# Optimization experiments

Hardware: AMD Instinct MI355X
Metric: run time of the kernel (lower is better)

## Reference

```python
import jax, jax.numpy as jnp
import numpy as np

N_USERS = 100_000
N_ENTITIES = 200_000
N_EDGES = 1_000_000
NNZ = 1_000_000
C = 64          # embedding dim
N_FACTORS = 4
N_REL_M1 = 10   # n_relations - 1
N_HOPS = 2
TEMP = 0.2


def setup_inputs() -> dict:
    key = jax.random.key(0)
    ks = jax.random.split(key, 10)
    return {
        'user_emb': jax.random.normal(ks[0], (N_USERS, C), jnp.float32) * 0.1,
        'entity_emb': jax.random.normal(ks[1], (N_ENTITIES, C), jnp.float32) * 0.1,
        'latent_emb': jax.random.normal(ks[2], (N_FACTORS, C), jnp.float32) * 0.1,
        'weight': jax.random.normal(ks[3], (N_REL_M1, C), jnp.float32) * 0.1,
        'disen_weight_att': jax.random.normal(ks[4], (N_FACTORS, N_REL_M1), jnp.float32) * 0.1,
        'edge_index': jax.random.randint(ks[5], (2, N_EDGES), 0, N_ENTITIES, dtype=jnp.int32),
        'edge_type': jax.random.randint(ks[6], (N_EDGES,), 1, N_REL_M1 + 1, dtype=jnp.int32),
        'inter_rows': jax.random.randint(ks[7], (NNZ,), 0, N_USERS, dtype=jnp.int32),
        'inter_cols': jax.random.randint(ks[8], (NNZ,), 0, N_ENTITIES, dtype=jnp.int32),
        'inter_vals': jax.random.uniform(ks[9], (NNZ,), jnp.float32),
    }


def _l2norm(x):
    # F.normalize(x, dim=1) with eps=1e-12
    n = jnp.linalg.norm(x, axis=1, keepdims=True)
    return x / jnp.maximum(n, 1e-12)


def _mutual_information(disen_weight_att):
    disen_T = disen_weight_att.T                                    # [R-1, F]
    nd = disen_T / jnp.linalg.norm(disen_T, axis=1, keepdims=True)
    pos_scores = jnp.sum(nd * nd, axis=1)
    ttl_scores = jnp.sum(disen_T @ disen_weight_att, axis=1)
    pos = jnp.exp(pos_scores / TEMP)
    ttl = jnp.exp(ttl_scores / TEMP)
    return -jnp.sum(jnp.log(pos / ttl))


def reference(user_emb, entity_emb, latent_emb, weight, disen_weight_att,
              edge_index, edge_type, inter_rows, inter_cols, inter_vals):
    entity_res = entity_emb
    user_res = user_emb
    cor = _mutual_information(disen_weight_att)

    head, tail = edge_index[0], edge_index[1]
    # edge degree for scatter_mean (constant across hops)
    cnt = jax.ops.segment_sum(jnp.ones((N_EDGES,), jnp.float32), head,
                              num_segments=N_ENTITIES)
    inv_cnt = 1.0 / jnp.maximum(cnt, 1.0)

    for _ in range(N_HOPS):
        # KG aggregate: gather tail entities, modulate by relation, scatter-mean to head
        rel = weight[edge_type - 1]                                  # [E, C]
        neigh = entity_emb[tail] * rel                               # [E, C]
        entity_agg = jax.ops.segment_sum(neigh, head, num_segments=N_ENTITIES)
        entity_agg = entity_agg * inv_cnt[:, None]

        # user -> latent factor attention
        score = jax.nn.softmax(user_emb @ latent_emb.T, axis=1)[:, :, None]  # [U, F, 1]

        # sparse user aggregate: interact_mat @ entity_emb
        user_agg = jax.ops.segment_sum(inter_vals[:, None] * entity_emb[inter_cols],
                                       inter_rows, num_segments=N_USERS)     # [U, C]

        disen_weight = jax.nn.softmax(disen_weight_att, axis=-1) @ weight    # [F, C]
        user_agg = user_agg * jnp.sum(disen_weight[None] * score, axis=1) + user_agg

        entity_emb = _l2norm(entity_agg)
        user_emb = _l2norm(user_agg)
        entity_res = entity_res + entity_emb
        user_res = user_res + user_emb

    return entity_res, user_res, cor
```

## Files before the change

kernel.cpp:

```cpp
#include <hip/hip_runtime.h>
#include <math.h>

#define N_USERS    100000
#define N_ENTITIES 200000
#define N_EDGES    1000000
#define NNZ        1000000
#define CDIM       64
#define N_FACTORS  4
#define N_REL      10
#define TEMP       0.2f

#define CB         1024
#define NBE        196
#define NBU        98
#define CAPE       8192
#define CAPU       12288
#define ACHUNK     4096
#define GA         245
#define GCVT       6250
#define KG_BLOCKS  6250
#define USER_BLOCKS 3125
#define PCHUNK     4096
#define GPE        49
#define GPU_       25

typedef unsigned int u32;
typedef unsigned short u16;
typedef unsigned char u8;

#if defined(__has_builtin)
#if __has_builtin(__builtin_amdgcn_cvt_pk_f32_fp8) && __has_builtin(__builtin_amdgcn_cvt_pk_fp8_f32)
#define HAVE_HW_FP8 1
#endif
#endif

__device__ __forceinline__ float bflo(u32 w) { return __uint_as_float(w << 16); }
__device__ __forceinline__ float bfhi(u32 w) { return __uint_as_float(w & 0xFFFF0000u); }
__device__ __forceinline__ u16 f2bf(float f) {
    u32 u = __float_as_uint(f);
    u32 r = u + 0x7FFFu + ((u >> 16) & 1u);
    return (u16)(r >> 16);
}
__device__ __forceinline__ void unpack8_bf(uint4 rv, float* x) {
    x[0] = bflo(rv.x); x[1] = bfhi(rv.x);
    x[2] = bflo(rv.y); x[3] = bfhi(rv.y);
    x[4] = bflo(rv.z); x[5] = bfhi(rv.z);
    x[6] = bflo(rv.w); x[7] = bfhi(rv.w);
}
__device__ __forceinline__ uint4 pack8_bf(const float* x) {
    uint4 o;
    o.x = (u32)f2bf(x[0]) | ((u32)f2bf(x[1]) << 16);
    o.y = (u32)f2bf(x[2]) | ((u32)f2bf(x[3]) << 16);
    o.z = (u32)f2bf(x[4]) | ((u32)f2bf(x[5]) << 16);
    o.w = (u32)f2bf(x[6]) | ((u32)f2bf(x[7]) << 16);
    return o;
}

#ifndef HAVE_HW_FP8
__device__ __forceinline__ float fp8_dec1(u32 b) {
    u32 s = b >> 7, em = b & 0x7F;
    float mag;
    if (em < 8) mag = (float)em * 0.001953125f;
    else {
        u32 bits = (((em >> 3) + 120u) << 23) | ((em & 7u) << 20);
        mag = __uint_as_float(bits);
    }
    return s ? -mag : mag;
}
__device__ __forceinline__ u32 fp8_enc1(float f) {
    float a = fabsf(f);
    u32 s = (__float_as_uint(f) >> 31) << 7;
    if (a < 0.015625f) {
        int n = (int)rintf(a * 512.0f);
        return s | (u32)n;
    }
    u32 u = __float_as_uint(a);
    u32 r = u + 0x0007FFFFu + ((u >> 20) & 1u);
    int ee = (int)((r >> 23) & 0xFF) - 127 + 7;
    if (ee >= 16) return s | 0x7Eu;
    return s | ((u32)ee << 3) | ((r >> 20) & 7u);
}
#endif

__device__ __forceinline__ void unpack8_fp8(uint2 rv, float* x) {
#ifdef HAVE_HW_FP8
    typedef float floatx2 __attribute__((ext_vector_type(2)));
    floatx2 a0 = __builtin_amdgcn_cvt_pk_f32_fp8(rv.x, false);
    floatx2 a1 = __builtin_amdgcn_cvt_pk_f32_fp8(rv.x, true);
    floatx2 a2 = __builtin_amdgcn_cvt_pk_f32_fp8(rv.y, false);
    floatx2 a3 = __builtin_amdgcn_cvt_pk_f32_fp8(rv.y, true);
    x[0] = a0.x; x[1] = a0.y; x[2] = a1.x; x[3] = a1.y;
    x[4] = a2.x; x[5] = a2.y; x[6] = a3.x; x[7] = a3.y;
#else
    x[0] = fp8_dec1(rv.x & 0xFF);         x[1] = fp8_dec1((rv.x >> 8) & 0xFF);
    x[2] = fp8_dec1((rv.x >> 16) & 0xFF); x[3] = fp8_dec1(rv.x >> 24);
    x[4] = fp8_dec1(rv.y & 0xFF);         x[5] = fp8_dec1((rv.y >> 8) & 0xFF);
    x[6] = fp8_dec1((rv.y >> 16) & 0xFF); x[7] = fp8_dec1(rv.y >> 24);
#endif
}
__device__ __forceinline__ uint2 pack8_fp8(const float* x) {
    uint2 o;
#ifdef HAVE_HW_FP8
    int v0 = 0, v1 = 0;
    v0 = __builtin_amdgcn_cvt_pk_fp8_f32(x[0], x[1], v0, false);
    v0 = __builtin_amdgcn_cvt_pk_fp8_f32(x[2], x[3], v0, true);
    v1 = __builtin_amdgcn_cvt_pk_fp8_f32(x[4], x[5], v1, false);
    v1 = __builtin_amdgcn_cvt_pk_fp8_f32(x[6], x[7], v1, true);
    o.x = (u32)v0; o.y = (u32)v1;
#else
    o.x = fp8_enc1(x[0]) | (fp8_enc1(x[1]) << 8) | (fp8_enc1(x[2]) << 16) | (fp8_enc1(x[3]) << 24);
    o.y = fp8_enc1(x[4]) | (fp8_enc1(x[5]) << 8) | (fp8_enc1(x[6]) << 16) | (fp8_enc1(x[7]) << 24);
#endif
    return o;
}

__device__ __forceinline__ void fma_rowW(float* acc, uint2 rv, int rel,
                                         const float* __restrict__ weight, int seg) {
    float x[8]; unpack8_fp8(rv, x);
    const float4* wp = (const float4*)(weight + rel * CDIM + seg * 8);
    float4 w0 = wp[0], w1 = wp[1];
    acc[0] += x[0] * w0.x; acc[1] += x[1] * w0.y;
    acc[2] += x[2] * w0.z; acc[3] += x[3] * w0.w;
    acc[4] += x[4] * w1.x; acc[5] += x[5] * w1.y;
    acc[6] += x[6] * w1.z; acc[7] += x[7] * w1.w;
}
__device__ __forceinline__ void fma_rowV(float* acc, uint2 rv, float v) {
    float x[8]; unpack8_fp8(rv, x);
    #pragma unroll
    for (int k = 0; k < 8; ++k) acc[k] += v * x[k];
}

__device__ void dev_cvt(int b, const float* __restrict__ in, u8* __restrict__ out) {
    int i = b * 256 + threadIdx.x;
    const float4* p = (const float4*)(in + (size_t)i * 8);
    float4 a = p[0], bb = p[1];
    float x[8] = {a.x, a.y, a.z, a.w, bb.x, bb.y, bb.z, bb.w};
    *(uint2*)(out + (size_t)i * 8) = pack8_fp8(x);
}

__device__ void dev_bin_edges(int b, const int* __restrict__ head,
                              const int* __restrict__ tail, const int* __restrict__ etype,
                              int* __restrict__ zcur, int* __restrict__ binbuf) {
    __shared__ int lh[256], lbase[256];
    int t = threadIdx.x;
    lh[t] = 0; __syncthreads();
    int base = b * ACHUNK;
    int rec[16], rnk[16], bkt[16];
    #pragma unroll
    for (int k = 0; k < 16; ++k) {
        int i = base + k * 256 + t;
        rnk[k] = -1; rec[k] = 0; bkt[k] = 0;
        if (i < N_EDGES) {
            int h = head[i];
            bkt[k] = h >> 10;
            rec[k] = ((h & 1023) << 22) | ((etype[i] - 1) << 18) | tail[i];
            rnk[k] = atomicAdd(&lh[bkt[k]], 1);
        }
    }
    __syncthreads();
    lbase[t] = lh[t] ? (t * CAPE + atomicAdd(&zcur[t], lh[t])) : 0;
    __syncthreads();
    #pragma unroll
    for (int k = 0; k < 16; ++k)
        if (rnk[k] >= 0) binbuf[lbase[bkt[k]] + rnk[k]] = rec[k];
}

__device__ void dev_bin_inter(int b, const int* __restrict__ rows,
                              const int* __restrict__ cols, const float* __restrict__ vals,
                              int* __restrict__ zcur, int2* __restrict__ binbuf) {
    __shared__ int lh[256], lbase[256];
    int t = threadIdx.x;
    lh[t] = 0; __syncthreads();
    int base = b * ACHUNK;
    int recx[16], recy[16], rnk[16], bkt[16];
    #pragma unroll
    for (int k = 0; k < 16; ++k) {
        int i = base + k * 256 + t;
        rnk[k] = -1; recx[k] = 0; recy[k] = 0; bkt[k] = 0;
        if (i < NNZ) {
            int r = rows[i];
            bkt[k] = r >> 10;
            recx[k] = ((r & 1023) << 18) | cols[i];
            recy[k] = __float_as_int(vals[i]);
            rnk[k] = atomicAdd(&lh[bkt[k]], 1);
        }
    }
    __syncthreads();
    lbase[t] = lh[t] ? (t * CAPU + atomicAdd(&zcur[t], lh[t])) : 0;
    __syncthreads();
    #pragma unroll
    for (int k = 0; k < 16; ++k)
        if (rnk[k] >= 0) {
            int2 p; p.x = recx[k]; p.y = recy[k];
            binbuf[lbase[bkt[k]] + rnk[k]] = p;
        }
}

__device__ void dev_disen_cor(const float* __restrict__ att,
                              const float* __restrict__ weight,
                              float* __restrict__ dw, float* __restrict__ cor_out) {
    int tid = threadIdx.x;
    int f = tid >> 6, c = tid & 63;
    float m = -1e30f;
    for (int r = 0; r < N_REL; ++r) m = fmaxf(m, att[f * N_REL + r]);
    float e[N_REL], s = 0.0f;
    for (int r = 0; r < N_REL; ++r) { e[r] = __expf(att[f * N_REL + r] - m); s += e[r]; }
    float acc = 0.0f;
    for (int r = 0; r < N_REL; ++r) acc += (e[r] / s) * weight[r * CDIM + c];
    dw[f * CDIM + c] = acc;

    if (tid == 0) {
        float rowsum[N_FACTORS];
        for (int ff = 0; ff < N_FACTORS; ++ff) {
            float ss = 0.0f;
            for (int j = 0; j < N_REL; ++j) ss += att[ff * N_REL + j];
            rowsum[ff] = ss;
        }
        float cor = 0.0f;
        for (int i = 0; i < N_REL; ++i) {
            float nsq = 0.0f, ttl = 0.0f;
            for (int ff = 0; ff < N_FACTORS; ++ff) {
                float a = att[ff * N_REL + i];
                nsq += a * a;
                ttl += a * rowsum[ff];
            }
            float n = sqrtf(nsq);
            float pos = 0.0f;
            for (int ff = 0; ff < N_FACTORS; ++ff) {
                float a = att[ff * N_REL + i] / n;
                pos += a * a;
            }
            cor += (ttl - pos) / TEMP;
        }
        *cor_out = cor;
    }
}

__global__ __launch_bounds__(256) void prep_kernel(const float* __restrict__ entity_emb,
                                                   u8* __restrict__ ef8,
                                                   const int* __restrict__ head,
                                                   const int* __restrict__ tail,
                                                   const int* __restrict__ etype,
                                                   const int* __restrict__ rows,
                                                   const int* __restrict__ cols,
                                                   const float* __restrict__ vals,
                                                   int* __restrict__ zce, int* __restrict__ zcu,
                                                   int* __restrict__ bine, int2* __restrict__ binu,
                                                   const float* __restrict__ att,
                                                   const float* __restrict__ weight,
                                                   float* __restrict__ dw,
                                                   float* __restrict__ cor_out) {
    int bid = blockIdx.x;
    if (bid < GCVT)                 dev_cvt(bid, entity_emb, ef8);
    else if (bid < GCVT + GA)       dev_bin_edges(bid - GCVT, head, tail, etype, zce, bine);
    else if (bid < GCVT + 2 * GA)   dev_bin_inter(bid - GCVT - GA, rows, cols, vals, zcu, binu);
    else                            dev_disen_cor(att, weight, dw, cor_out);
}

__device__ void dev_build_e(int b, const int* __restrict__ zce,
                            const int* __restrict__ binbuf,
                            int2* __restrict__ einfo, int* __restrict__ epk,
                            int* __restrict__ dbinE) {
    __shared__ int lh[CB];
    __shared__ int ss[256];
    __shared__ int ldeg[64];
    int t = threadIdx.x;
    int bstart = b * CAPE;
    int bend = bstart + zce[b];
    #pragma unroll
    for (int k = 0; k < 4; ++k) lh[t * 4 + k] = 0;
    if (t < 64) ldeg[t] = 0;
    __syncthreads();
    for (int j = bstart + t; j < bend; j += 256)
        atomicAdd(&lh[(u32)binbuf[j] >> 22], 1);
    __syncthreads();
    int v[4], acc = 0;
    #pragma unroll
    for (int k = 0; k < 4; ++k) { v[k] = lh[t * 4 + k]; acc += v[k]; }
    ss[t] = acc; __syncthreads();
    #pragma unroll
    for (int d = 1; d < 256; d <<= 1) {
        int x = (t >= d) ? ss[t - d] : 0;
        __syncthreads();
        ss[t] += x;
        __syncthreads();
    }
    int excl = ss[t] - acc;
    int hbase = b * CB;
    #pragma unroll
    for (int k = 0; k < 4; ++k) {
        int hl = t * 4 + k;
        int h = hbase + hl;
        if (h < N_ENTITIES) {
            int2 inf; inf.x = bstart + excl; inf.y = v[k];
            einfo[h] = inf;
            atomicAdd(&ldeg[63 - min(v[k], 63)], 1);
        }
        lh[hl] = excl;
        excl += v[k];
    }
    __syncthreads();
    if (t < 64 && ldeg[t]) atomicAdd(&dbinE[t], ldeg[t]);
    for (int j = bstart + t; j < bend; j += 256) {
        int rec = binbuf[j];
        int pos = atomicAdd(&lh[(u32)rec >> 22], 1);
        epk[bstart + pos] = rec & 0x3FFFFF;
    }
}

__device__ void dev_build_u(int b, const int* __restrict__ zcu,
                            const int2* __restrict__ binbuf,
                            int2* __restrict__ uinfo, int2* __restrict__ ucv,
                            int* __restrict__ dbinU) {
    __shared__ int lh[CB];
    __shared__ int ss[256];
    __shared__ int ldeg[64];
    int t = threadIdx.x;
    int bstart = b * CAPU;
    int bend = bstart + zcu[b];
    #pragma unroll
    for (int k = 0; k < 4; ++k) lh[t * 4 + k] = 0;
    if (t < 64) ldeg[t] = 0;
    __syncthreads();
    for (int j = bstart + t; j < bend; j += 256)
        atomicAdd(&lh[(u32)binbuf[j].x >> 18], 1);
    __syncthreads();
    int v[4], acc = 0;
    #pragma unroll
    for (int k = 0; k < 4; ++k) { v[k] = lh[t * 4 + k]; acc += v[k]; }
    ss[t] = acc; __syncthreads();
    #pragma unroll
    for (int d = 1; d < 256; d <<= 1) {
        int x = (t >= d) ? ss[t - d] : 0;
        __syncthreads();
        ss[t] += x;
        __syncthreads();
    }
    int excl = ss[t] - acc;
    int ubase = b * CB;
    #pragma unroll
    for (int k = 0; k < 4; ++k) {
        int ul = t * 4 + k;
        int u = ubase + ul;
        if (u < N_USERS) {
            int2 inf; inf.x = bstart + excl; inf.y = v[k];
            uinfo[u] = inf;
            atomicAdd(&ldeg[63 - min(v[k], 63)], 1);
        }
        lh[ul] = excl;
        excl += v[k];
    }
    __syncthreads();
    if (t < 64 && ldeg[t]) atomicAdd(&dbinU[t], ldeg[t]);
    for (int j = bstart + t; j < bend; j += 256) {
        int2 rec = binbuf[j];
        int pos = atomicAdd(&lh[(u32)rec.x >> 18], 1);
        int2 out; out.x = rec.x & 0x3FFFF; out.y = rec.y;
        ucv[bstart + pos] = out;
    }
}

__global__ __launch_bounds__(256) void build_kernel(const int* __restrict__ zce,
                                                    const int* __restrict__ zcu,
                                                    const int* __restrict__ bine,
                                                    const int2* __restrict__ binu,
                                                    int2* __restrict__ einfo, int* __restrict__ epk,
                                                    int2* __restrict__ uinfo, int2* __restrict__ ucv,
                                                    int* __restrict__ dbinE, int* __restrict__ dbinU) {
    int bid = blockIdx.x;
    if (bid < NBE) dev_build_e(bid, zce, bine, einfo, epk, dbinE);
    else           dev_build_u(bid - NBE, zcu, binu, uinfo, ucv, dbinU);
}

__device__ void dev_perm(int b, int n, const int2* __restrict__ info,
                         const int* __restrict__ dbin,
                         int* __restrict__ zdeg, int2* __restrict__ perm) {
    __shared__ int dbase[64], dtmp[64];
    __shared__ int lh[64], lbase[64];
    int t = threadIdx.x;
    if (t < 64) { dtmp[t] = dbin[t]; lh[t] = 0; }
    __syncthreads();
    if (t < 64) {
        int v = dtmp[t];
        #pragma unroll
        for (int d = 1; d < 64; d <<= 1) {
            int x = (t >= d) ? dtmp[t - d] : 0;
            __syncthreads();
            dtmp[t] += x;
            __syncthreads();
        }
        dbase[t] = dtmp[t] - v;
    } else {
        #pragma unroll
        for (int d = 1; d < 64; d <<= 1) { __syncthreads(); __syncthreads(); }
    }
    __syncthreads();
    int base = b * PCHUNK;
    int rnk[16], bin[16], deg[16], st[16];
    #pragma unroll
    for (int k = 0; k < 16; ++k) {
        int i = base + k * 256 + t;
        rnk[k] = -1;
        if (i < n) {
            int2 q = info[i];
            deg[k] = q.y; st[k] = q.x;
            bin[k] = 63 - min(deg[k], 63);
            rnk[k] = atomicAdd(&lh[bin[k]], 1);
        }
    }
    __syncthreads();
    if (t < 64) lbase[t] = lh[t] ? (dbase[t] + atomicAdd(&zdeg[t], lh[t])) : 0;
    __syncthreads();
    #pragma unroll
    for (int k = 0; k < 16; ++k)
        if (rnk[k] >= 0) {
            int i = base + k * 256 + t;
            int2 p;
            p.x = (int)(((u32)min(deg[k], 16383) << 18) | (u32)i);
            p.y = st[k];
            perm[lbase[bin[k]] + rnk[k]] = p;
        }
}

__global__ __launch_bounds__(256) void perm_kernel(const int2* __restrict__ einfo,
                                                   const int2* __restrict__ uinfo,
                                                   const int* __restrict__ dbinE,
                                                   const int* __restrict__ dbinU,
                                                   int* __restrict__ zdegE, int* __restrict__ zdegU,
                                                   int2* __restrict__ permE, int2* __restrict__ permU) {
    int bid = blockIdx.x;
    if (bid < GPE) dev_perm(bid, N_ENTITIES, einfo, dbinE, zdegE, permE);
    else           dev_perm(bid - GPE, N_USERS, uinfo, dbinU, zdegU, permU);
}

__device__ void dev_kg_hop(int widg, const u8* __restrict__ esrc,
                           const int2* __restrict__ permE,
                           const int* __restrict__ epk,
                           const float* __restrict__ weight,
                           const float* __restrict__ emb0,
                           u8* __restrict__ enew, float* __restrict__ eres, int last) {
    int lane = threadIdx.x & 63;
    int slot = lane >> 3, seg = lane & 7;
    int2 pe = permE[widg * 8 + slot];
    u32 px = (u32)pe.x;
    int d = px >> 18, h = (int)(px & 0x3FFFFu), s = pe.y;
    int dmax = __shfl(d, (lane & 7), 64);

    float acc[8];
    #pragma unroll
    for (int k = 0; k < 8; ++k) acc[k] = 0.0f;
    const uint2 uz = make_uint2(0u, 0u);

    for (int it = 0; it < dmax; it += 4) {
        int pk[4]; uint2 rv[4];
        #pragma unroll
        for (int q = 0; q < 4; ++q)
            pk[q] = (it + q < d) ? epk[s + it + q] : 0;
        #pragma unroll
        for (int q = 0; q < 4; ++q)
            rv[q] = (it + q < d)
                  ? *(const uint2*)(esrc + (size_t)(pk[q] & 0x3FFFF) * CDIM + seg * 8) : uz;
        #pragma unroll
        for (int q = 0; q < 4; ++q)
            fma_rowW(acc, rv[q], pk[q] >> 18, weight, seg);
    }
    float inv = 1.0f / fmaxf((float)d, 1.0f);
    float ssq = 0.0f;
    #pragma unroll
    for (int k = 0; k < 8; ++k) { acc[k] *= inv; ssq += acc[k] * acc[k]; }
    ssq += __shfl_xor(ssq, 1, 64);
    ssq += __shfl_xor(ssq, 2, 64);
    ssq += __shfl_xor(ssq, 4, 64);
    float rn = 1.0f / fmaxf(sqrtf(ssq), 1e-12f);
    #pragma unroll
    for (int k = 0; k < 8; ++k) acc[k] *= rn;

    size_t base = (size_t)h * CDIM + seg * 8;
    if (!last) {
        *(uint2*)(enew + base) = pack8_fp8(acc);
    } else {
        uint2 pv = *(const uint2*)(esrc + base);
        float o0[8]; unpack8_fp8(pv, o0);
        float4 a = *(const float4*)(emb0 + base);
        float4 b = *(const float4*)(emb0 + base + 4);
        float4 r0, r1;
        r0.x = a.x + o0[0] + acc[0]; r0.y = a.y + o0[1] + acc[1];
        r0.z = a.z + o0[2] + acc[2]; r0.w = a.w + o0[3] + acc[3];
        r1.x = b.x + o0[4] + acc[4]; r1.y = b.y + o0[5] + acc[5];
        r1.z = b.z + o0[6] + acc[6]; r1.w = b.w + o0[7] + acc[7];
        *(float4*)(eres + base) = r0;
        *(float4*)(eres + base + 4) = r1;
    }
}

__device__ void dev_user_hop(int widg, const float* __restrict__ uoldf,
                             const u16* __restrict__ uoldb,
                             const u8* __restrict__ esrc,
                             const int2* __restrict__ permU,
                             const int2* __restrict__ ucv,
                             const float* __restrict__ latent,
                             const float* __restrict__ dw,
                             const float* __restrict__ uemb0,
                             u16* __restrict__ unew, float* __restrict__ ures, int last) {
    int lane = threadIdx.x & 63;
    int slot = lane >> 3, seg = lane & 7;
    int2 pe = permU[widg * 8 + slot];
    u32 px = (u32)pe.x;
    int d = px >> 18, u = (int)(px & 0x3FFFFu), s = pe.y;
    int dmax = __shfl(d, (lane & 7), 64);

    float acc[8];
    #pragma unroll
    for (int k = 0; k < 8; ++k) acc[k] = 0.0f;
    const uint2 uz = make_uint2(0u, 0u);
    const int2 cz = make_int2(0, 0);

    for (int it = 0; it < dmax; it += 4) {
        int2 cc[4]; uint2 rv[4];
        #pragma unroll
        for (int q = 0; q < 4; ++q)
            cc[q] = (it + q < d) ? ucv[s + it + q] : cz;
        #pragma unroll
        for (int q = 0; q < 4; ++q)
            rv[q] = (it + q < d)
                  ? *(const uint2*)(esrc + (size_t)cc[q].x * CDIM + seg * 8) : uz;
        #pragma unroll
        for (int q = 0; q < 4; ++q)
            fma_rowV(acc, rv[q], __int_as_float(cc[q].y));
    }

    float uo[8];
    size_t ubase = (size_t)u * CDIM + seg * 8;
    if (uoldb) {
        uint4 pv = *(const uint4*)(uoldb + ubase);
        unpack8_bf(pv, uo);
    } else {
        float4 a = *(const float4*)(uoldf + ubase);
        float4 b = *(const float4*)(uoldf + ubase + 4);
        uo[0] = a.x; uo[1] = a.y; uo[2] = a.z; uo[3] = a.w;
        uo[4] = b.x; uo[5] = b.y; uo[6] = b.z; uo[7] = b.w;
    }
    float dts[N_FACTORS];
    #pragma unroll
    for (int f = 0; f < N_FACTORS; ++f) {
        const float4* lp = (const float4*)(latent + f * CDIM + seg * 8);
        float4 l0 = lp[0], l1 = lp[1];
        float p = uo[0] * l0.x + uo[1] * l0.y + uo[2] * l0.z + uo[3] * l0.w +
                  uo[4] * l1.x + uo[5] * l1.y + uo[6] * l1.z + uo[7] * l1.w;
        p += __shfl_xor(p, 1, 64);
        p += __shfl_xor(p, 2, 64);
        p += __shfl_xor(p, 4, 64);
        dts[f] = p;
    }
    float m = fmaxf(fmaxf(dts[0], dts[1]), fmaxf(dts[2], dts[3]));
    float e0 = __expf(dts[0] - m), e1 = __expf(dts[1] - m);
    float e2 = __expf(dts[2] - m), e3 = __expf(dts[3] - m);
    float inv_ssum = 1.0f / (e0 + e1 + e2 + e3);
    e0 *= inv_ssum; e1 *= inv_ssum; e2 *= inv_ssum; e3 *= inv_ssum;

    const float4* d0p = (const float4*)(dw + 0 * CDIM + seg * 8);
    const float4* d1p = (const float4*)(dw + 1 * CDIM + seg * 8);
    const float4* d2p = (const float4*)(dw + 2 * CDIM + seg * 8);
    const float4* d3p = (const float4*)(dw + 3 * CDIM + seg * 8);
    float4 ga0 = d0p[0], ga1 = d0p[1];
    float4 gb0 = d1p[0], gb1 = d1p[1];
    float4 gc0 = d2p[0], gc1 = d2p[1];
    float4 gd0 = d3p[0], gd1 = d3p[1];
    float g[8];
    g[0] = e0 * ga0.x + e1 * gb0.x + e2 * gc0.x + e3 * gd0.x;
    g[1] = e0 * ga0.y + e1 * gb0.y + e2 * gc0.y + e3 * gd0.y;
    g[2] = e0 * ga0.z + e1 * gb0.z + e2 * gc0.z + e3 * gd0.z;
    g[3] = e0 * ga0.w + e1 * gb0.w + e2 * gc0.w + e3 * gd0.w;
    g[4] = e0 * ga1.x + e1 * gb1.x + e2 * gc1.x + e3 * gd1.x;
    g[5] = e0 * ga1.y + e1 * gb1.y + e2 * gc1.y + e3 * gd1.y;
    g[6] = e0 * ga1.z + e1 * gb1.z + e2 * gc1.z + e3 * gd1.z;
    g[7] = e0 * ga1.w + e1 * gb1.w + e2 * gc1.w + e3 * gd1.w;

    float ssq = 0.0f;
    #pragma unroll
    for (int k = 0; k < 8; ++k) {
        acc[k] = acc[k] * (1.0f + g[k]);
        ssq += acc[k] * acc[k];
    }
    ssq += __shfl_xor(ssq, 1, 64);
    ssq += __shfl_xor(ssq, 2, 64);
    ssq += __shfl_xor(ssq, 4, 64);
    float rn = 1.0f / fmaxf(sqrtf(ssq), 1e-12f);
    #pragma unroll
    for (int k = 0; k < 8; ++k) acc[k] *= rn;

    if (!last) {
        *(uint4*)(unew + ubase) = pack8_bf(acc);
    } else {
        float4 a = *(const float4*)(uemb0 + ubase);
        float4 b = *(const float4*)(uemb0 + ubase + 4);
        float4 r0, r1;
        r0.x = a.x + uo[0] + acc[0]; r0.y = a.y + uo[1] + acc[1];
        r0.z = a.z + uo[2] + acc[2]; r0.w = a.w + uo[3] + acc[3];
        r1.x = b.x + uo[4] + acc[4]; r1.y = b.y + uo[5] + acc[5];
        r1.z = b.z + uo[6] + acc[6]; r1.w = b.w + uo[7] + acc[7];
        *(float4*)(ures + ubase) = r0;
        *(float4*)(ures + ubase + 4) = r1;
    }
}

__global__ __launch_bounds__(256, 8) void hop_kernel(const u8* __restrict__ e_src,
                                                  const int2* __restrict__ permE,
                                                  const int* __restrict__ epk,
                                                  const float* __restrict__ weight,
                                                  const float* __restrict__ entity_emb,
                                                  u8* __restrict__ eA,
                                                  float* __restrict__ eres,
                                                  const float* __restrict__ uoldf,
                                                  const u16* __restrict__ uoldb,
                                                  const int2* __restrict__ permU,
                                                  const int2* __restrict__ ucv,
                                                  const float* __restrict__ latent,
                                                  const float* __restrict__ dw,
                                                  const float* __restrict__ user_emb,
                                                  u16* __restrict__ uA,
                                                  float* __restrict__ ures,
                                                  int last) {
    int bid = blockIdx.x;
    int wave = threadIdx.x >> 6;
    if (bid < USER_BLOCKS) {
        dev_user_hop(bid * 4 + wave, uoldf, uoldb, e_src, permU, ucv,
                     latent, dw, user_emb, uA, ures, last);
    } else {
        dev_kg_hop((bid - USER_BLOCKS) * 4 + wave, e_src, permE, epk, weight,
                   entity_emb, eA, eres, last);
    }
}

static inline size_t align16(size_t x) { return (x + 15) & ~(size_t)15; }

extern "C" void kernel_launch(void* const* d_in, const int* in_sizes, int n_in,
                              void* d_out, int out_size, void* d_ws, size_t ws_size,
                              hipStream_t stream) {
    const float* user_emb   = (const float*)d_in[0];
    const float* entity_emb = (const float*)d_in[1];
    const float* latent_emb = (const float*)d_in[2];
    const float* weight     = (const float*)d_in[3];
    const float* att        = (const float*)d_in[4];
    const int*   edge_index = (const int*)d_in[5];
    const int*   edge_type  = (const int*)d_in[6];
    const int*   inter_rows = (const int*)d_in[7];
    const int*   inter_cols = (const int*)d_in[8];
    const float* inter_vals = (const float*)d_in[9];

    float* eres = (float*)d_out;
    float* ures = eres + (size_t)N_ENTITIES * CDIM;
    float* cor  = ures + (size_t)N_USERS * CDIM;

    char* ws = (char*)d_ws;
    u8*    ef8   = (u8*)ws;   ws += align16(sizeof(u8) * (size_t)N_ENTITIES * CDIM);
    u8*    eA    = (u8*)ws;   ws += align16(sizeof(u8) * (size_t)N_ENTITIES * CDIM);
    u16*   uA    = (u16*)ws;  ws += align16(sizeof(u16) * (size_t)N_USERS * CDIM);
    int*   epk   = (int*)ws;  ws += align16(sizeof(int) * (size_t)NBE * CAPE);
    int2*  ucv   = (int2*)ws; ws += align16(sizeof(int2) * (size_t)NBU * CAPU);
    int*   bine  = (int*)ws;  ws += align16(sizeof(int) * (size_t)NBE * CAPE);
    int2*  binu  = (int2*)ws; ws += align16(sizeof(int2) * (size_t)NBU * CAPU);
    int2*  einfo = (int2*)ws; ws += align16(sizeof(int2) * N_ENTITIES);
    int2*  uinfo = (int2*)ws; ws += align16(sizeof(int2) * N_USERS);
    int*   ctrs  = (int*)ws;  ws += align16(sizeof(int) * 768);
    int2*  permE = (int2*)ws; ws += align16(sizeof(int2) * N_ENTITIES);
    int2*  permU = (int2*)ws; ws += align16(sizeof(int2) * N_USERS);
    float* dw    = (float*)ws; ws += align16(sizeof(float) * N_FACTORS * CDIM);

    int* zce   = ctrs;
    int* zcu   = ctrs + 256;
    int* dbinE = ctrs + 512;
    int* dbinU = ctrs + 576;
    int* zdegE = ctrs + 640;
    int* zdegU = ctrs + 704;

    const int* head = edge_index;
    const int* tail = edge_index + N_EDGES;

    (void)hipMemsetAsync(ctrs, 0, sizeof(int) * 768, stream);

    prep_kernel<<<GCVT + 2 * GA + 1, 256, 0, stream>>>(
        entity_emb, ef8, head, tail, edge_type,
        inter_rows, inter_cols, inter_vals,
        zce, zcu, bine, binu, att, weight, dw, cor);
    build_kernel<<<NBE + NBU, 256, 0, stream>>>(zce, zcu, bine, binu,
                                                einfo, epk, uinfo, ucv, dbinE, dbinU);
    perm_kernel<<<GPE + GPU_, 256, 0, stream>>>(einfo, uinfo, dbinE, dbinU,
                                                zdegE, zdegU, permE, permU);

    hop_kernel<<<USER_BLOCKS + KG_BLOCKS, 256, 0, stream>>>(
        ef8, permE, epk, weight, entity_emb, eA, eres,
        user_emb, (const u16*)nullptr, permU, ucv, latent_emb, dw, user_emb, uA, ures, 0);
    hop_kernel<<<USER_BLOCKS + KG_BLOCKS, 256, 0, stream>>>(
        eA, permE, epk, weight, entity_emb, (u8*)nullptr, eres,
        (const float*)nullptr, uA, permU, ucv, latent_emb, dw, user_emb, (u16*)nullptr, ures, 1);
}
```

Before: 201.6 us.

## Fold degree-sorted permutation into build kernel with per-block local sorting

Result: slower. 233.6 us (+15.9%).

```diff
diff --git a/kernel.cpp b/kernel.cpp
--- a/kernel.cpp
+++ b/kernel.cpp
@@ -18,11 +18,8 @@
 #define ACHUNK     4096
 #define GA         245
 #define GCVT       6250
-#define KG_BLOCKS  6250
-#define USER_BLOCKS 3125
-#define PCHUNK     4096
-#define GPE        49
-#define GPU_       25
+#define KG_BLOCKS2   6272
+#define USER_BLOCKS2 3136
 
 typedef unsigned int u32;
 typedef unsigned short u16;
@@ -259,17 +256,17 @@
 
 __device__ void dev_build_e(int b, const int* __restrict__ zce,
                             const int* __restrict__ binbuf,
-                            int2* __restrict__ einfo, int* __restrict__ epk,
-                            int* __restrict__ dbinE) {
+                            int* __restrict__ epk, int2* __restrict__ perm) {
     __shared__ int lh[CB];
     __shared__ int ss[256];
-    __shared__ int ldeg[64];
+    __shared__ int lbs[64];
+    __shared__ int lhist[64];
     int t = threadIdx.x;
     int bstart = b * CAPE;
     int bend = bstart + zce[b];
     #pragma unroll
     for (int k = 0; k < 4; ++k) lh[t * 4 + k] = 0;
-    if (t < 64) ldeg[t] = 0;
+    if (t < 64) lhist[t] = 0;
     __syncthreads();
     for (int j = bstart + t; j < bend; j += 256)
         atomicAdd(&lh[(u32)binbuf[j] >> 22], 1);
@@ -287,20 +284,40 @@
     }
     int excl = ss[t] - acc;
     int hbase = b * CB;
+    int st[4], dg[4], vld[4];
     #pragma unroll
     for (int k = 0; k < 4; ++k) {
         int hl = t * 4 + k;
         int h = hbase + hl;
-        if (h < N_ENTITIES) {
-            int2 inf; inf.x = bstart + excl; inf.y = v[k];
-            einfo[h] = inf;
-            atomicAdd(&ldeg[63 - min(v[k], 63)], 1);
-        }
+        vld[k] = (h < N_ENTITIES);
+        st[k] = bstart + excl;
+        dg[k] = v[k];
+        if (vld[k]) atomicAdd(&lhist[63 - min(v[k], 63)], 1);
         lh[hl] = excl;
         excl += v[k];
     }
-    __syncthreads();
-    if (t < 64 && ldeg[t]) atomicAdd(&dbinE[t], ldeg[t]);
+    #pragma unroll
+    for (int k = 0; k < 4; ++k) {
+        int2 sent; sent.x = 0x3FFFF; sent.y = 0;
+        perm[hbase + t * 4 + k] = sent;
+    }
+    __syncthreads();
+    if (t == 0) {
+        int run = 0;
+        for (int bb = 0; bb < 64; ++bb) { lbs[bb] = run; run += lhist[bb]; lhist[bb] = 0; }
+    }
+    __syncthreads();
+    #pragma unroll
+    for (int k = 0; k < 4; ++k) {
+        if (vld[k]) {
+            int bin = 63 - min(dg[k], 63);
+            int pos = lbs[bin] + atomicAdd(&lhist[bin], 1);
+            int2 p;
+            p.x = (int)(((u32)min(dg[k], 16383) << 18) | (u32)(hbase + t * 4 + k));
+            p.y = st[k];
+            perm[hbase + pos] = p;
+        }
+    }
     for (int j = bstart + t; j < bend; j += 256) {
         int rec = binbuf[j];
         int pos = atomicAdd(&lh[(u32)rec >> 22], 1);
@@ -310,17 +327,17 @@
 
 __device__ void dev_build_u(int b, const int* __restrict__ zcu,
                             const int2* __restrict__ binbuf,
-                            int2* __restrict__ uinfo, int2* __restrict__ ucv,
-                            int* __restrict__ dbinU) {
+                            int2* __restrict__ ucv, int2* __restrict__ perm) {
     __shared__ int lh[CB];
     __shared__ int ss[256];
-    __shared__ int ldeg[64];
+    __shared__ int lbs[64];
+    __shared__ int lhist[64];
     int t = threadIdx.x;
     int bstart = b * CAPU;
     int bend = bstart + zcu[b];
     #pragma unroll
     for (int k = 0; k < 4; ++k) lh[t * 4 + k] = 0;
-    if (t < 64) ldeg[t] = 0;
+    if (t < 64) lhist[t] = 0;
     __syncthreads();
     for (int j = bstart + t; j < bend; j += 256)
         atomicAdd(&lh[(u32)binbuf[j].x >> 18], 1);
@@ -338,20 +355,40 @@
     }
     int excl = ss[t] - acc;
     int ubase = b * CB;
+    int st[4], dg[4], vld[4];
     #pragma unroll
     for (int k = 0; k < 4; ++k) {
         int ul = t * 4 + k;
         int u = ubase + ul;
-        if (u < N_USERS) {
-            int2 inf; inf.x = bstart + excl; inf.y = v[k];
-            uinfo[u] = inf;
-            atomicAdd(&ldeg[63 - min(v[k], 63)], 1);
-        }
+        vld[k] = (u < N_USERS);
+        st[k] = bstart + excl;
+        dg[k] = v[k];
+        if (vld[k]) atomicAdd(&lhist[63 - min(v[k], 63)], 1);
         lh[ul] = excl;
         excl += v[k];
     }
-    __syncthreads();
-    if (t < 64 && ldeg[t]) atomicAdd(&dbinU[t], ldeg[t]);
+    #pragma unroll
+    for (int k = 0; k < 4; ++k) {
+        int2 sent; sent.x = 0x3FFFF; sent.y = 0;
+        perm[ubase + t * 4 + k] = sent;
+    }
+    __syncthreads();
+    if (t == 0) {
+        int run = 0;
+        for (int bb = 0; bb < 64; ++bb) { lbs[bb] = run; run += lhist[bb]; lhist[bb] = 0; }
+    }
+    __syncthreads();
+    #pragma unroll
+    for (int k = 0; k < 4; ++k) {
+        if (vld[k]) {
+            int bin = 63 - min(dg[k], 63);
+            int pos = lbs[bin] + atomicAdd(&lhist[bin], 1);
+            int2 p;
+            p.x = (int)(((u32)min(dg[k], 16383) << 18) | (u32)(ubase + t * 4 + k));
+            p.y = st[k];
+            perm[ubase + pos] = p;
+        }
+    }
     for (int j = bstart + t; j < bend; j += 256) {
         int2 rec = binbuf[j];
         int pos = atomicAdd(&lh[(u32)rec.x >> 18], 1);
@@ -364,73 +401,13 @@
                                                     const int* __restrict__ zcu,
                                                     const int* __restrict__ bine,
                                                     const int2* __restrict__ binu,
-                                                    int2* __restrict__ einfo, int* __restrict__ epk,
-                                                    int2* __restrict__ uinfo, int2* __restrict__ ucv,
-                                                    int* __restrict__ dbinE, int* __restrict__ dbinU) {
+                                                    int* __restrict__ epk,
+                                                    int2* __restrict__ ucv,
+                                                    int2* __restrict__ permE,
+                                                    int2* __restrict__ permU) {
     int bid = blockIdx.x;
-    if (bid < NBE) dev_build_e(bid, zce, bine, einfo, epk, dbinE);
-    else           dev_build_u(bid - NBE, zcu, binu, uinfo, ucv, dbinU);
-}
-
-__device__ void dev_perm(int b, int n, const int2* __restrict__ info,
-                         const int* __restrict__ dbin,
-                         int* __restrict__ zdeg, int2* __restrict__ perm) {
-    __shared__ int dbase[64], dtmp[64];
-    __shared__ int lh[64], lbase[64];
-    int t = threadIdx.x;
-    if (t < 64) { dtmp[t] = dbin[t]; lh[t] = 0; }
-    __syncthreads();
-    if (t < 64) {
-        int v = dtmp[t];
-        #pragma unroll
-        for (int d = 1; d < 64; d <<= 1) {
-            int x = (t >= d) ? dtmp[t - d] : 0;
-            __syncthreads();
-            dtmp[t] += x;
-            __syncthreads();
-        }
-        dbase[t] = dtmp[t] - v;
-    } else {
-        #pragma unroll
-        for (int d = 1; d < 64; d <<= 1) { __syncthreads(); __syncthreads(); }
-    }
-    __syncthreads();
-    int base = b * PCHUNK;
-    int rnk[16], bin[16], deg[16], st[16];
-    #pragma unroll
-    for (int k = 0; k < 16; ++k) {
-        int i = base + k * 256 + t;
-        rnk[k] = -1;
-        if (i < n) {
-            int2 q = info[i];
-            deg[k] = q.y; st[k] = q.x;
-            bin[k] = 63 - min(deg[k], 63);
-            rnk[k] = atomicAdd(&lh[bin[k]], 1);
-        }
-    }
-    __syncthreads();
-    if (t < 64) lbase[t] = lh[t] ? (dbase[t] + atomicAdd(&zdeg[t], lh[t])) : 0;
-    __syncthreads();
-    #pragma unroll
-    for (int k = 0; k < 16; ++k)
-        if (rnk[k] >= 0) {
-            int i = base + k * 256 + t;
-            int2 p;
-            p.x = (int)(((u32)min(deg[k], 16383) << 18) | (u32)i);
-            p.y = st[k];
-            perm[lbase[bin[k]] + rnk[k]] = p;
-        }
-}
-
-__global__ __launch_bounds__(256) void perm_kernel(const int2* __restrict__ einfo,
-                                                   const int2* __restrict__ uinfo,
-                                                   const int* __restrict__ dbinE,
-                                                   const int* __restrict__ dbinU,
-                                                   int* __restrict__ zdegE, int* __restrict__ zdegU,
-                                                   int2* __restrict__ permE, int2* __restrict__ permU) {
-    int bid = blockIdx.x;
-    if (bid < GPE) dev_perm(bid, N_ENTITIES, einfo, dbinE, zdegE, permE);
-    else           dev_perm(bid - GPE, N_USERS, uinfo, dbinU, zdegU, permU);
+    if (bid < NBE) dev_build_e(bid, zce, bine, epk, permE);
+    else           dev_build_u(bid - NBE, zcu, binu, ucv, permU);
 }
 
 __device__ void dev_kg_hop(int widg, const u8* __restrict__ esrc,
@@ -464,6 +441,7 @@
         for (int q = 0; q < 4; ++q)
             fma_rowW(acc, rv[q], pk[q] >> 18, weight, seg);
     }
+    if (h >= N_ENTITIES) return;
     float inv = 1.0f / fmaxf((float)d, 1.0f);
     float ssq = 0.0f;
     #pragma unroll
@@ -528,6 +506,7 @@
         for (int q = 0; q < 4; ++q)
             fma_rowV(acc, rv[q], __int_as_float(cc[q].y));
     }
+    if (u >= N_USERS) return;
 
     float uo[8];
     size_t ubase = (size_t)u * CDIM + seg * 8;
@@ -604,7 +583,7 @@
     }
 }
 
-__global__ __launch_bounds__(256, 8) void hop_kernel(const u8* __restrict__ e_src,
+__global__ __launch_bounds__(256) void hop_kernel(const u8* __restrict__ e_src,
                                                   const int2* __restrict__ permE,
                                                   const int* __restrict__ epk,
                                                   const float* __restrict__ weight,
@@ -623,11 +602,11 @@
                                                   int last) {
     int bid = blockIdx.x;
     int wave = threadIdx.x >> 6;
-    if (bid < USER_BLOCKS) {
+    if (bid < USER_BLOCKS2) {
         dev_user_hop(bid * 4 + wave, uoldf, uoldb, e_src, permU, ucv,
                      latent, dw, user_emb, uA, ures, last);
     } else {
-        dev_kg_hop((bid - USER_BLOCKS) * 4 + wave, e_src, permE, epk, weight,
+        dev_kg_hop((bid - USER_BLOCKS2) * 4 + wave, e_src, permE, epk, weight,
                    entity_emb, eA, eres, last);
     }
 }
@@ -660,38 +639,30 @@
     int2*  ucv   = (int2*)ws; ws += align16(sizeof(int2) * (size_t)NBU * CAPU);
     int*   bine  = (int*)ws;  ws += align16(sizeof(int) * (size_t)NBE * CAPE);
     int2*  binu  = (int2*)ws; ws += align16(sizeof(int2) * (size_t)NBU * CAPU);
-    int2*  einfo = (int2*)ws; ws += align16(sizeof(int2) * N_ENTITIES);
-    int2*  uinfo = (int2*)ws; ws += align16(sizeof(int2) * N_USERS);
-    int*   ctrs  = (int*)ws;  ws += align16(sizeof(int) * 768);
-    int2*  permE = (int2*)ws; ws += align16(sizeof(int2) * N_ENTITIES);
-    int2*  permU = (int2*)ws; ws += align16(sizeof(int2) * N_USERS);
+    int*   ctrs  = (int*)ws;  ws += align16(sizeof(int) * 512);
+    int2*  permE = (int2*)ws; ws += align16(sizeof(int2) * (size_t)NBE * CB);
+    int2*  permU = (int2*)ws; ws += align16(sizeof(int2) * (size_t)NBU * CB);
     float* dw    = (float*)ws; ws += align16(sizeof(float) * N_FACTORS * CDIM);
 
-    int* zce   = ctrs;
-    int* zcu   = ctrs + 256;
-    int* dbinE = ctrs + 512;
-    int* dbinU = ctrs + 576;
-    int* zdegE = ctrs + 640;
-    int* zdegU = ctrs + 704;
+    int* zce = ctrs;
+    int* zcu = ctrs + 256;
 
     const int* head = edge_index;
     const int* tail = edge_index + N_EDGES;
 
-    (void)hipMemsetAsync(ctrs, 0, sizeof(int) * 768, stream);
+    (void)hipMemsetAsync(ctrs, 0, sizeof(int) * 512, stream);
 
     prep_kernel<<<GCVT + 2 * GA + 1, 256, 0, stream>>>(
         entity_emb, ef8, head, tail, edge_type,
         inter_rows, inter_cols, inter_vals,
         zce, zcu, bine, binu, att, weight, dw, cor);
     build_kernel<<<NBE + NBU, 256, 0, stream>>>(zce, zcu, bine, binu,
-                                                einfo, epk, uinfo, ucv, dbinE, dbinU);
-    perm_kernel<<<GPE + GPU_, 256, 0, stream>>>(einfo, uinfo, dbinE, dbinU,
-                                                zdegE, zdegU, permE, permU);
-
-    hop_kernel<<<USER_BLOCKS + KG_BLOCKS, 256, 0, stream>>>(
+                                                epk, ucv, permE, permU);
+
+    hop_kernel<<<USER_BLOCKS2 + KG_BLOCKS2, 256, 0, stream>>>(
         ef8, permE, epk, weight, entity_emb, eA, eres,
         user_emb, (const u16*)nullptr, permU, ucv, latent_emb, dw, user_emb, uA, ures, 0);
-    hop_kernel<<<USER_BLOCKS + KG_BLOCKS, 256, 0, stream>>>(
+    hop_kernel<<<USER_BLOCKS2 + KG_BLOCKS2, 256, 0, stream>>>(
         eA, permE, epk, weight, entity_emb, (u8*)nullptr, eres,
         (const float*)nullptr, uA, permU, ucv, latent_emb, dw, user_emb, (u16*)nullptr, ures, 1);
 }
```
